# Kernel optimization log

Measured on AMD Instinct MI355X. Metric: run time of the kernel, lower is better.

## Reference

```python
import jax, jax.numpy as jnp
import numpy as np

N_EMBD = 1024
N_HEAD = 16

def setup_inputs() -> dict:
    key = jax.random.key(0)
    ks = jax.random.split(key, 6)
    C = N_EMBD
    s = 1.0 / np.sqrt(C)
    x = jax.random.normal(ks[0], (4, 2048, C), dtype=jnp.float32)
    Wk = jax.random.normal(ks[1], (C, C), dtype=jnp.float32) * s
    Wq = jax.random.normal(ks[2], (C, C), dtype=jnp.float32) * s
    Wv = jax.random.normal(ks[3], (C, C), dtype=jnp.float32) * s
    Wp = jax.random.normal(ks[4], (C, C), dtype=jnp.float32) * s
    bp = jax.random.normal(ks[5], (C,), dtype=jnp.float32) * 0.01
    return {"x": x, "Wq": Wq, "Wk": Wk, "Wv": Wv, "Wp": Wp, "bp": bp}

def reference(x, Wq, Wk, Wv, Wp, bp):
    B, T, C = x.shape
    H = N_HEAD
    d = C // H
    # projections (bias=False)
    q = (x @ Wq).reshape(B, T, H, d).transpose(0, 2, 1, 3)  # [B,H,T,d]
    k = (x @ Wk).reshape(B, T, H, d).transpose(0, 2, 1, 3)
    v = (x @ Wv).reshape(B, T, H, d).transpose(0, 2, 1, 3)
    att = jnp.einsum('bhqd,bhkd->bhqk', q, k) * (1.0 / np.sqrt(d))
    causal = jnp.tril(jnp.ones((T, T), dtype=bool))
    att = jnp.where(causal[None, None], att, jnp.float32(-jnp.inf))
    att = jax.nn.softmax(att, axis=-1)
    y = jnp.einsum('bhqk,bhkd->bhqd', att, v)  # [B,H,T,d]
    y = y.transpose(0, 2, 1, 3).reshape(B, T, C)
    return y @ Wp + bp
```

## Files before the change

### kernel.cpp

```cpp
#include <hip/hip_runtime.h>
#include <hip/hip_bf16.h>

#define N_EMBD 1024
#define N_HEADS 16
#define HD 64
#define TSEQ 2048
#define BATCH 4
#define M_TOT (BATCH*TSEQ)

typedef short s16x8 __attribute__((ext_vector_type(8)));
typedef float f32x4 __attribute__((ext_vector_type(4)));

__device__ __forceinline__ void glds16(const void* g, void* l) {
  __builtin_amdgcn_global_load_lds((const __attribute__((address_space(1))) void*)g,
                                   (__attribute__((address_space(3))) void*)l, 16, 0, 0);
}

__device__ __forceinline__ float exp_scaled(float s) {
  float r;
  asm("v_exp_f32 %0, %1\n\ts_nop 0" : "=v"(r) : "v"(s * 0.18033688011112042f));
  return r;
}

__device__ __forceinline__ unsigned cvtpk(float lo, float hi) {
  unsigned r;
  asm("v_cvt_pk_bf16_f32 %0, %1, %2" : "=v"(r) : "v"(lo), "v"(hi));
  return r;
}

__global__ __launch_bounds__(256) void xcast_kernel(const float* __restrict__ x,
                                                    __hip_bfloat16* __restrict__ xb) {
  int i = blockIdx.x * 256 + threadIdx.x;
  float4 f = ((const float4*)x)[i];
  __hip_bfloat162 p0, p1;
  p0.x = __float2bfloat16(f.x); p0.y = __float2bfloat16(f.y);
  p1.x = __float2bfloat16(f.z); p1.y = __float2bfloat16(f.w);
  ((__hip_bfloat162*)xb)[2*i]   = p0;
  ((__hip_bfloat162*)xb)[2*i+1] = p1;
}

__global__ void wcast_kernel(const float* __restrict__ Wq, const float* __restrict__ Wk,
                             const float* __restrict__ Wv, const float* __restrict__ Wp,
                             __hip_bfloat16* __restrict__ wqkvt, __hip_bfloat16* __restrict__ wpt) {
  __shared__ float tile[32][33];
  int z = blockIdx.z;
  const float* in = (z==0)?Wq:(z==1)?Wk:(z==2)?Wv:Wp;
  __hip_bfloat16* out = (z<3) ? (wqkvt + (size_t)z*N_EMBD*N_EMBD) : wpt;
  int tx = threadIdx.x, ty = threadIdx.y;
  int x  = blockIdx.x*32 + tx;
  int y0 = blockIdx.y*32;
  #pragma unroll
  for (int j=0;j<4;++j) tile[ty + j*8][tx] = in[(size_t)(y0+ty+j*8)*N_EMBD + x];
  __syncthreads();
  int xo  = y0 + tx;
  int yo0 = blockIdx.x*32;
  #pragma unroll
  for (int j=0;j<4;++j)
    out[(size_t)(yo0+ty+j*8)*N_EMBD + xo] = __float2bfloat16(tile[tx][ty+j*8]);
}

__global__ __launch_bounds__(256) void gemm_kernel(
    const __hip_bfloat16* __restrict__ A,
    const __hip_bfloat16* __restrict__ Bt,
    __hip_bfloat16* __restrict__ Qb, __hip_bfloat16* __restrict__ Kb,
    __hip_bfloat16* __restrict__ Vt,
    float* __restrict__ out, const float* __restrict__ bias, int mode) {
  __shared__ __align__(16) char smem[32768];
  __hip_bfloat16* Alin = (__hip_bfloat16*)smem;
  __hip_bfloat16* Blin = (__hip_bfloat16*)(smem + 16384);
  int tid = threadIdx.x;
  int m0 = blockIdx.y*128, n0 = blockIdx.x*128;
  int w = tid>>6, lane = tid&63, l16 = lane&15, quad = lane>>4;
  int wr = w>>1, wc = w&1;
  int xg = l16 & 7;
  int off0 = ((quad    ) ^ xg)*8;
  int off1 = ((quad + 4) ^ xg)*8;
  f32x4 acc[4][4];
  #pragma unroll
  for (int mi=0;mi<4;++mi)
    #pragma unroll
    for (int ni=0;ni<4;++ni) acc[mi][ni] = (f32x4){0.f,0.f,0.f,0.f};

  for (int k0=0; k0<N_EMBD; k0+=64) {
    __syncthreads();
    #pragma unroll
    for (int rd=0; rd<4; ++rd) {
      int slot = rd*256 + tid;
      int row  = slot>>3;
      int gc8  = ((tid&7) ^ (row&7))*8;
      glds16(A  + (size_t)(m0+row)*N_EMBD + k0 + gc8, Alin + slot*8);
      glds16(Bt + (size_t)(n0+row)*N_EMBD + k0 + gc8, Blin + slot*8);
    }
    __syncthreads();
    #pragma unroll
    for (int c=0;c<2;++c) {
      int off = c ? off1 : off0;
      s16x8 af[4], bfr[4];
      #pragma unroll
      for (int mi=0;mi<4;++mi)
        af[mi] = *(const s16x8*)(Alin + (wr*64+mi*16+l16)*64 + off);
      #pragma unroll
      for (int ni=0;ni<4;++ni)
        bfr[ni] = *(const s16x8*)(Blin + (wc*64+ni*16+l16)*64 + off);
      #pragma unroll
      for (int mi=0;mi<4;++mi)
        #pragma unroll
        for (int ni=0;ni<4;++ni)
          acc[mi][ni] = __builtin_amdgcn_mfma_f32_16x16x32_bf16(af[mi], bfr[ni], acc[mi][ni],0,0,0);
    }
  }

  if (mode == 0) {
    int which = n0 >> 10;
    int bb = m0 >> 11, t0 = m0 & 2047;
    if (which < 2) {
      __hip_bfloat16* outp = (which==0)?Qb:Kb;
      #pragma unroll
      for (int mi=0;mi<4;++mi) {
        #pragma unroll
        for (int ni=0;ni<4;++ni) {
          int ncol = (n0 & 1023) + wc*64 + ni*16 + l16;
          int hh = ncol>>6, dd = ncol&63;
          #pragma unroll
          for (int r=0;r<4;++r) {
            int t = t0 + wr*64 + mi*16 + quad*4 + r;
            outp[((size_t)(bb*N_HEADS + hh)*TSEQ + t)*HD + dd] = __float2bfloat16(acc[mi][ni][r]);
          }
        }
      }
    } else {
      int hh0 = (n0 & 1023) >> 6;
      __hip_bfloat16 (*Ts)[136] = (__hip_bfloat16(*)[136])smem;
      #pragma unroll
      for (int p=0;p<2;++p) {
        __syncthreads();
        if (wc == p) {
          #pragma unroll
          for (int mi=0;mi<4;++mi)
            #pragma unroll
            for (int ni=0;ni<4;++ni) {
              int dd = ni*16 + l16;
              #pragma unroll
              for (int r=0;r<4;++r)
                Ts[dd][wr*64 + mi*16 + quad*4 + r] = __float2bfloat16(acc[mi][ni][r]);
            }
        }
        __syncthreads();
        int dd = tid>>2, tc = (tid&3)*32;
        __hip_bfloat16* dst = Vt + ((size_t)(bb*N_HEADS + hh0 + p)*HD + dd)*TSEQ + t0;
        #pragma unroll
        for (int pb=0; pb<8; ++pb) {
          int q  = tc + pb*4;
          int pp = q & 63;
          int key = (q & 64) | (pp & 32) | ((pp & 4) << 2) | ((pp & 24) >> 1);
          *(uint2*)(dst + q) = *(const uint2*)&Ts[dd][key];
        }
      }
    }
  } else {
    #pragma unroll
    for (int mi=0;mi<4;++mi) {
      #pragma unroll
      for (int ni=0;ni<4;++ni) {
        int col = n0 + wc*64 + ni*16 + l16;
        float bs = bias[col];
        #pragma unroll
        for (int r=0;r<4;++r) {
          int m = m0 + wr*64 + mi*16 + quad*4 + r;
          out[(size_t)m*N_EMBD + col] = acc[mi][ni][r] + bs;
        }
      }
    }
  }
}

__global__ __launch_bounds__(256) void attn_kernel(
    const __hip_bfloat16* __restrict__ Qb, const __hip_bfloat16* __restrict__ Kb,
    const __hip_bfloat16* __restrict__ Vt, __hip_bfloat16* __restrict__ Yb) {
  __shared__ __align__(16) __hip_bfloat16 Ks[2][64][64];
  __shared__ __align__(16) __hip_bfloat16 Vs[2][64][64];
  int tid = threadIdx.x;
  int wgid = blockIdx.x;
  int qb = (int)((0x01237564AB89CDEFull >> ((wgid>>6)*4)) & 15);
  int h  = (wgid>>2) & 15;
  int b  = wgid & 3;
  int q0 = qb*128;
  size_t bhT  = (size_t)(b*N_HEADS + h)*TSEQ;
  size_t bhHD = (size_t)(b*N_HEADS + h)*HD;
  int lane = tid&63, w = tid>>6, l16 = lane&15, quad = lane>>4;
  int wq = w*32;
  int xg = l16 & 7;
  int off0 = ((quad    ) ^ xg)*8;
  int off1 = ((quad + 4) ^ xg)*8;

  int slot0 = tid,        row0 = slot0>>3, gcA = ((tid&7) ^ (row0&7))*8;
  int slot1 = 256 + tid,  row1 = slot1>>3, gcB = ((tid&7) ^ (row1&7))*8;

  s16x8 qf[2][2];
  #pragma unroll
  for (int mi=0;mi<2;++mi) {
    const __hip_bfloat16* qrow = Qb + (bhT + q0 + wq + mi*16 + l16)*HD;
    qf[mi][0] = *(const s16x8*)(qrow + quad*8);
    qf[mi][1] = *(const s16x8*)(qrow + 32 + quad*8);
  }

  f32x4 z4 = {0.f,0.f,0.f,0.f};
  f32x4 oacc[4][2];
  #pragma unroll
  for (int nd=0;nd<4;++nd) { oacc[nd][0]=z4; oacc[nd][1]=z4; }
  float lsum[2] = {0.f, 0.f};

  int ntiles = 2*qb + 2;

  {
    glds16(Kb + (bhT + 0 + row0)*HD + gcA,    &Ks[0][0][0] + slot0*8);
    glds16(Vt + (bhHD + row0)*TSEQ + 0 + gcA, &Vs[0][0][0] + slot0*8);
    glds16(Kb + (bhT + 0 + row1)*HD + gcB,    &Ks[0][0][0] + slot1*8);
    glds16(Vt + (bhHD + row1)*TSEQ + 0 + gcB, &Vs[0][0][0] + slot1*8);
  }

  for (int t=0; t<ntiles; ++t) {
    int cur = t&1;
    int k0 = t*64;
    if (t+1 < ntiles) {
      int kn = k0 + 64;
      glds16(Kb + (bhT + kn + row0)*HD + gcA,     &Ks[cur^1][0][0] + slot0*8);
      glds16(Vt + (bhHD + row0)*TSEQ + kn + gcA,  &Vs[cur^1][0][0] + slot0*8);
      glds16(Kb + (bhT + kn + row1)*HD + gcB,     &Ks[cur^1][0][0] + slot1*8);
      glds16(Vt + (bhHD + row1)*TSEQ + kn + gcB,  &Vs[cur^1][0][0] + slot1*8);
      asm volatile("s_waitcnt vmcnt(4)" ::: "memory");
    } else {
      asm volatile("s_waitcnt vmcnt(0)" ::: "memory");
    }
    __builtin_amdgcn_s_barrier();
    __builtin_amdgcn_sched_barrier(0);

    const __hip_bfloat16* Kc = &Ks[cur][0][0];
    const __hip_bfloat16* Vc = &Vs[cur][0][0];

    f32x4 sacc[4][2];
    #pragma unroll
    for (int ni=0; ni<4; ++ni) {
      s16x8 kb0 = *(const s16x8*)(Kc + (ni*16+l16)*64 + off0);
      s16x8 kb1 = *(const s16x8*)(Kc + (ni*16+l16)*64 + off1);
      #pragma unroll
      for (int mi=0; mi<2; ++mi) {
        f32x4 s = z4;
        s = __builtin_amdgcn_mfma_f32_16x16x32_bf16(kb0, qf[mi][0], s,0,0,0);
        s = __builtin_amdgcn_mfma_f32_16x16x32_bf16(kb1, qf[mi][1], s,0,0,0);
        sacc[ni][mi] = s;
      }
    }

    unsigned pkw[2][4][2];
    if (q0 + wq >= k0 + 63) {
      #pragma unroll
      for (int ni=0; ni<4; ++ni) {
        #pragma unroll
        for (int mi=0; mi<2; ++mi) {
          float e0 = exp_scaled(sacc[ni][mi][0]);
          float e1 = exp_scaled(sacc[ni][mi][1]);
          float e2 = exp_scaled(sacc[ni][mi][2]);
          float e3 = exp_scaled(sacc[ni][mi][3]);
          lsum[mi] += (e0+e1)+(e2+e3);
          pkw[mi][ni][0] = cvtpk(e0, e1);
          pkw[mi][ni][1] = cvtpk(e2, e3);
        }
      }
    } else {
      #pragma unroll
      for (int ni=0; ni<4; ++ni) {
        int kbase = k0 + ni*16 + quad*4;
        #pragma unroll
        for (int mi=0; mi<2; ++mi) {
          int qrow = q0 + wq + mi*16 + l16;
          float e0 = (qrow >= kbase    ) ? exp_scaled(sacc[ni][mi][0]) : 0.f;
          float e1 = (qrow >= kbase + 1) ? exp_scaled(sacc[ni][mi][1]) : 0.f;
          float e2 = (qrow >= kbase + 2) ? exp_scaled(sacc[ni][mi][2]) : 0.f;
          float e3 = (qrow >= kbase + 3) ? exp_scaled(sacc[ni][mi][3]) : 0.f;
          lsum[mi] += (e0+e1)+(e2+e3);
          pkw[mi][ni][0] = cvtpk(e0, e1);
          pkw[mi][ni][1] = cvtpk(e2, e3);
        }
      }
    }

    union U8 { s16x8 v; unsigned u[4]; };
    U8 pf[2][2];
    #pragma unroll
    for (int c=0; c<2; ++c)
      #pragma unroll
      for (int mi=0; mi<2; ++mi) {
        pf[c][mi].u[0] = pkw[mi][2*c  ][0];
        pf[c][mi].u[1] = pkw[mi][2*c  ][1];
        pf[c][mi].u[2] = pkw[mi][2*c+1][0];
        pf[c][mi].u[3] = pkw[mi][2*c+1][1];
      }
    #pragma unroll
    for (int nd=0; nd<4; ++nd) {
      const __hip_bfloat16* vrow = Vc + (nd*16 + l16)*64;
      s16x8 vb0 = *(const s16x8*)(vrow + off0);
      s16x8 vb1 = *(const s16x8*)(vrow + off1);
      oacc[nd][0] = __builtin_amdgcn_mfma_f32_16x16x32_bf16(vb0, pf[0][0].v, oacc[nd][0],0,0,0);
      oacc[nd][1] = __builtin_amdgcn_mfma_f32_16x16x32_bf16(vb0, pf[0][1].v, oacc[nd][1],0,0,0);
      oacc[nd][0] = __builtin_amdgcn_mfma_f32_16x16x32_bf16(vb1, pf[1][0].v, oacc[nd][0],0,0,0);
      oacc[nd][1] = __builtin_amdgcn_mfma_f32_16x16x32_bf16(vb1, pf[1][1].v, oacc[nd][1],0,0,0);
    }

    asm volatile("s_waitcnt lgkmcnt(0)" ::: "memory");
    __builtin_amdgcn_s_barrier();
    __builtin_amdgcn_sched_barrier(0);
  }

  #pragma unroll
  for (int mi=0; mi<2; ++mi) {
    lsum[mi] += __shfl_xor(lsum[mi], 16);
    lsum[mi] += __shfl_xor(lsum[mi], 32);
  }

  #pragma unroll
  for (int mi=0; mi<2; ++mi) {
    float inv = 1.f / lsum[mi];
    int tq = q0 + wq + mi*16 + l16;
    __hip_bfloat16* yr = Yb + ((size_t)(b*TSEQ + tq))*N_EMBD + h*HD + quad*4;
    #pragma unroll
    for (int nd=0; nd<4; ++nd) {
      uint2 o;
      o.x = cvtpk(oacc[nd][mi][0]*inv, oacc[nd][mi][1]*inv);
      o.y = cvtpk(oacc[nd][mi][2]*inv, oacc[nd][mi][3]*inv);
      *(uint2*)(yr + nd*16) = o;
    }
  }
}

extern "C" void kernel_launch(void* const* d_in, const int* in_sizes, int n_in,
                              void* d_out, int out_size, void* d_ws, size_t ws_size,
                              hipStream_t stream) {
  const float* x  = (const float*)d_in[0];
  const float* Wq = (const float*)d_in[1];
  const float* Wk = (const float*)d_in[2];
  const float* Wv = (const float*)d_in[3];
  const float* Wp = (const float*)d_in[4];
  const float* bp = (const float*)d_in[5];

  char* w = (char*)d_ws;
  __hip_bfloat16* xb    = (__hip_bfloat16*)w;  w += (size_t)M_TOT*N_EMBD*2;
  __hip_bfloat16* wqkvt = (__hip_bfloat16*)w;  w += (size_t)3*N_EMBD*N_EMBD*2;
  __hip_bfloat16* wpt   = (__hip_bfloat16*)w;  w += (size_t)N_EMBD*N_EMBD*2;
  __hip_bfloat16* Qb    = (__hip_bfloat16*)w;  w += (size_t)M_TOT*N_EMBD*2;
  __hip_bfloat16* Kb    = (__hip_bfloat16*)w;  w += (size_t)M_TOT*N_EMBD*2;
  __hip_bfloat16* Vt    = (__hip_bfloat16*)w;  w += (size_t)M_TOT*N_EMBD*2;
  __hip_bfloat16* Yb    = (__hip_bfloat16*)w;

  xcast_kernel<<<dim3(M_TOT*N_EMBD/1024), dim3(256), 0, stream>>>(x, xb);
  wcast_kernel<<<dim3(32,32,4), dim3(32,8), 0, stream>>>(Wq,Wk,Wv,Wp,wqkvt,wpt);
  gemm_kernel<<<dim3(24,64), dim3(256), 0, stream>>>(xb, wqkvt, Qb,Kb,Vt, nullptr, nullptr, 0);
  attn_kernel<<<dim3(1024), dim3(256), 0, stream>>>(Qb,Kb,Vt,Yb);
  gemm_kernel<<<dim3(8,64), dim3(256), 0, stream>>>(Yb, wpt, nullptr,nullptr,nullptr,
                                                    (float*)d_out, bp, 1);
}
```

Before: 239.2 us.

## Remap GEMM blocks per XCD and stage Q/K epilogue through LDS

Blocks are renumbered so that consecutive workgroups, which the hardware spreads round-robin over the eight XCDs, map to contiguous N-column ranges on each XCD. The aim is better L2 reuse of the B operand. The Q/K epilogue now transposes the accumulator tile through shared memory and writes 16-byte vectorized rows, replacing scattered 2-byte stores. This adds two barriers per head half, and the remap assumes gridDim.x is divisible by 8.

```diff
diff --git a/kernel.cpp b/kernel.cpp
--- a/kernel.cpp
+++ b/kernel.cpp
@@ -69,7 +69,12 @@
   __hip_bfloat16* Alin = (__hip_bfloat16*)smem;
   __hip_bfloat16* Blin = (__hip_bfloat16*)(smem + 16384);
   int tid = threadIdx.x;
-  int m0 = blockIdx.y*128, n0 = blockIdx.x*128;
+  int wg  = blockIdx.x + gridDim.x*blockIdx.y;
+  int per = gridDim.x >> 3;
+  int xcd = wg & 7, idx = wg >> 3;
+  int bxn = xcd*per + (idx % per);
+  int byn = idx / per;
+  int m0 = byn*128, n0 = bxn*128;
   int w = tid>>6, lane = tid&63, l16 = lane&15, quad = lane>>4;
   int wr = w>>1, wc = w&1;
   int xg = l16 & 7;
@@ -115,18 +120,29 @@
     int bb = m0 >> 11, t0 = m0 & 2047;
     if (which < 2) {
       __hip_bfloat16* outp = (which==0)?Qb:Kb;
-      #pragma unroll
-      for (int mi=0;mi<4;++mi) {
-        #pragma unroll
-        for (int ni=0;ni<4;++ni) {
-          int ncol = (n0 & 1023) + wc*64 + ni*16 + l16;
-          int hh = ncol>>6, dd = ncol&63;
+      int hh0 = (n0 & 1023) >> 6;
+      __hip_bfloat16 (*Tq)[68] = (__hip_bfloat16(*)[68])smem;
+      #pragma unroll
+      for (int p=0;p<2;++p) {
+        __syncthreads();
+        if (wc == p) {
           #pragma unroll
-          for (int r=0;r<4;++r) {
-            int t = t0 + wr*64 + mi*16 + quad*4 + r;
-            outp[((size_t)(bb*N_HEADS + hh)*TSEQ + t)*HD + dd] = __float2bfloat16(acc[mi][ni][r]);
-          }
-        }
+          for (int mi=0;mi<4;++mi)
+            #pragma unroll
+            for (int ni=0;ni<4;++ni) {
+              int col = ni*16 + l16;
+              int rbase = wr*64 + mi*16 + quad*4;
+              #pragma unroll
+              for (int r=0;r<4;++r)
+                Tq[rbase + r][col] = __float2bfloat16(acc[mi][ni][r]);
+            }
+        }
+        __syncthreads();
+        int row = tid>>1, half = (tid&1)*32;
+        __hip_bfloat16* dst = outp + ((size_t)(bb*N_HEADS + hh0 + p)*TSEQ + t0 + row)*HD + half;
+        #pragma unroll
+        for (int c4=0;c4<4;++c4)
+          *(uint4*)(dst + c4*8) = *(const uint4*)&Tq[row][half + c4*8];
       }
     } else {
       int hh0 = (n0 & 1023) >> 6;
```

Result: slower. 246.1 us (+2.9%).

## Add 256x256-tile double-buffered QKV GEMM kernel with 8 waves

Applied to the files above, without the earlier changes.

Replaces the 128x128-tile QKV projection GEMM with a new kernel that computes 256x256 output tiles using 512 threads. It double-buffers 128 KB of LDS, prefetches with global_load_lds interleaved across four quadrant MFMA phases, and uses explicit waitcnt, barriers and setprio. The larger tile raises arithmetic intensity and overlaps loads with compute. In exchange, LDS use caps occupancy at one block per CU and the grid shrinks to 384 blocks. The Q/K/V scatter epilogues are ported to the new tile shape and removed from the old kernel.

```diff
diff --git a/kernel.cpp b/kernel.cpp
--- a/kernel.cpp
+++ b/kernel.cpp
@@ -57,6 +57,172 @@
   #pragma unroll
   for (int j=0;j<4;++j)
     out[(size_t)(yo0+ty+j*8)*N_EMBD + xo] = __float2bfloat16(tile[tx][ty+j*8]);
+}
+
+__global__ __launch_bounds__(512, 2) void gemm256_kernel(
+    const __hip_bfloat16* __restrict__ A,
+    const __hip_bfloat16* __restrict__ Bt,
+    __hip_bfloat16* __restrict__ Qb, __hip_bfloat16* __restrict__ Kb,
+    __hip_bfloat16* __restrict__ Vt) {
+  __shared__ __align__(16) char smem[131072];
+  int tid = threadIdx.x;
+  int nb = blockIdx.x;
+  int m0 = blockIdx.y * 256;
+  const __hip_bfloat16* Asrc = A  + (size_t)m0 * N_EMBD;
+  const __hip_bfloat16* Bsrc = Bt + (size_t)nb * 256 * N_EMBD;
+
+  int lane = tid & 63, wv = tid >> 6, l16 = lane & 15, quad = lane >> 4;
+  int swr = wv >> 2, swc = wv & 3;
+  int xg = l16 & 7;
+  int offc0 = ((quad    ) ^ xg) * 8;
+  int offc1 = ((quad + 4) ^ xg) * 8;
+  int r0  = tid >> 3;
+  int gsw = ((tid & 7) ^ (r0 & 7)) * 8;
+  int gln = (tid & 7) * 8;
+
+  f32x4 acc[2][2][4][2];
+  #pragma unroll
+  for (int a=0;a<2;++a)
+    #pragma unroll
+    for (int b=0;b<2;++b)
+      #pragma unroll
+      for (int c=0;c<4;++c)
+        #pragma unroll
+        for (int d=0;d<2;++d) acc[a][b][c][d] = (f32x4){0.f,0.f,0.f,0.f};
+
+#define STG(srcbase, kk, hh_, dst_) do {                                      \
+    const __hip_bfloat16* s_ = (srcbase) + (size_t)((hh_)*128 + r0)*N_EMBD + (kk) + gsw; \
+    __hip_bfloat16* d_ = (dst_) + (hh_)*8192 + r0*64 + gln;                   \
+    glds16(s_, d_);                                                           \
+    glds16(s_ + (size_t)64*N_EMBD, d_ + 64*64);                               \
+  } while (0)
+#define RDA(qm_) do { _Pragma("unroll") for (int mi=0;mi<4;++mi) {            \
+    const __hip_bfloat16* p_ = Acur + ((qm_)*128 + swr*64 + mi*16 + l16)*64;  \
+    af[mi][0] = *(const s16x8*)(p_ + offc0);                                  \
+    af[mi][1] = *(const s16x8*)(p_ + offc1); } } while (0)
+#define RDB(qn_) do { _Pragma("unroll") for (int ni=0;ni<2;++ni) {            \
+    const __hip_bfloat16* p_ = Bcur + ((qn_)*128 + swc*32 + ni*16 + l16)*64;  \
+    bq[ni][0] = *(const s16x8*)(p_ + offc0);                                  \
+    bq[ni][1] = *(const s16x8*)(p_ + offc1); } } while (0)
+#define MM(qm_,qn_) do { _Pragma("unroll") for (int mi=0;mi<4;++mi)           \
+    _Pragma("unroll") for (int ni=0;ni<2;++ni) {                              \
+      acc[qm_][qn_][mi][ni] = __builtin_amdgcn_mfma_f32_16x16x32_bf16(af[mi][0], bq[ni][0], acc[qm_][qn_][mi][ni],0,0,0); \
+      acc[qm_][qn_][mi][ni] = __builtin_amdgcn_mfma_f32_16x16x32_bf16(af[mi][1], bq[ni][1], acc[qm_][qn_][mi][ni],0,0,0); } } while (0)
+
+  {
+    __hip_bfloat16* A0b = (__hip_bfloat16*)smem;
+    __hip_bfloat16* B0b = (__hip_bfloat16*)(smem + 32768);
+    STG(Asrc, 0, 0, A0b);
+    STG(Bsrc, 0, 0, B0b);
+    STG(Asrc, 0, 1, A0b);
+    STG(Bsrc, 0, 1, B0b);
+  }
+
+  for (int t = 0; t < 16; ++t) {
+    int kn = t*64 + 64;
+    char* cb   = smem + (size_t)(t & 1) * 65536;
+    char* nbuf = smem + (size_t)((t + 1) & 1) * 65536;
+    const __hip_bfloat16* Acur = (const __hip_bfloat16*)cb;
+    const __hip_bfloat16* Bcur = (const __hip_bfloat16*)(cb + 32768);
+    __hip_bfloat16* An = (__hip_bfloat16*)nbuf;
+    __hip_bfloat16* Bn = (__hip_bfloat16*)(nbuf + 32768);
+    bool pf = (t < 15);
+    s16x8 af[4][2], bq[2][2];
+
+    if (pf) { STG(Asrc, kn, 0, An); asm volatile("s_waitcnt vmcnt(6)" ::: "memory"); }
+    else    {                       asm volatile("s_waitcnt vmcnt(4)" ::: "memory"); }
+    __builtin_amdgcn_s_barrier();
+    __builtin_amdgcn_sched_barrier(0);
+    RDA(0); RDB(0);
+    asm volatile("s_waitcnt lgkmcnt(0)" ::: "memory");
+    __builtin_amdgcn_sched_barrier(0);
+    __builtin_amdgcn_s_setprio(1); MM(0,0); __builtin_amdgcn_s_setprio(0);
+
+    if (pf) { STG(Bsrc, kn, 0, Bn); asm volatile("s_waitcnt vmcnt(6)" ::: "memory"); }
+    else    {                       asm volatile("s_waitcnt vmcnt(2)" ::: "memory"); }
+    __builtin_amdgcn_s_barrier();
+    __builtin_amdgcn_sched_barrier(0);
+    RDA(1);
+    asm volatile("s_waitcnt lgkmcnt(0)" ::: "memory");
+    __builtin_amdgcn_sched_barrier(0);
+    __builtin_amdgcn_s_setprio(1); MM(1,0); __builtin_amdgcn_s_setprio(0);
+
+    if (pf) { STG(Asrc, kn, 1, An); asm volatile("s_waitcnt vmcnt(6)" ::: "memory"); }
+    else    {                       asm volatile("s_waitcnt vmcnt(0)" ::: "memory"); }
+    __builtin_amdgcn_s_barrier();
+    __builtin_amdgcn_sched_barrier(0);
+    RDB(1);
+    asm volatile("s_waitcnt lgkmcnt(0)" ::: "memory");
+    __builtin_amdgcn_sched_barrier(0);
+    __builtin_amdgcn_s_setprio(1); MM(1,1); __builtin_amdgcn_s_setprio(0);
+
+    if (pf) STG(Bsrc, kn, 1, Bn);
+    RDA(0);
+    asm volatile("s_waitcnt lgkmcnt(0)" ::: "memory");
+    __builtin_amdgcn_s_barrier();
+    __builtin_amdgcn_sched_barrier(0);
+    __builtin_amdgcn_s_setprio(1); MM(0,1); __builtin_amdgcn_s_setprio(0);
+  }
+#undef STG
+#undef RDA
+#undef RDB
+#undef MM
+
+  int which = nb >> 2;
+  int bb = m0 >> 11, t0 = m0 & 2047;
+  if (which < 2) {
+    __hip_bfloat16* outp = (which==0)?Qb:Kb;
+    int nloc = (nb & 3) * 256;
+    #pragma unroll
+    for (int qm=0;qm<2;++qm)
+      #pragma unroll
+      for (int qn=0;qn<2;++qn)
+        #pragma unroll
+        for (int mi=0;mi<4;++mi)
+          #pragma unroll
+          for (int ni=0;ni<2;++ni) {
+            int col = nloc + qn*128 + swc*32 + ni*16 + l16;
+            int hh = col >> 6, dd = col & 63;
+            int trow = t0 + qm*128 + swr*64 + mi*16 + quad*4;
+            __hip_bfloat16* dst = outp + ((size_t)(bb*N_HEADS + hh)*TSEQ + trow)*HD + dd;
+            #pragma unroll
+            for (int r=0;r<4;++r)
+              dst[(size_t)r*HD] = __float2bfloat16(acc[qm][qn][mi][ni][r]);
+          }
+  } else {
+    int hh0 = (nb & 3) * 4;
+    __hip_bfloat16 (*Ts)[264] = (__hip_bfloat16(*)[264])smem;
+    #pragma unroll
+    for (int hd=0; hd<4; ++hd) {
+      if (hd) __builtin_amdgcn_s_barrier();
+      if ((swc >> 1) == (hd & 1)) {
+        int qn = hd >> 1;
+        int ddb = (swc & 1) * 32;
+        #pragma unroll
+        for (int qm=0;qm<2;++qm)
+          #pragma unroll
+          for (int mi=0;mi<4;++mi)
+            #pragma unroll
+            for (int ni=0;ni<2;++ni) {
+              int dd = ddb + ni*16 + l16;
+              int trow = qm*128 + swr*64 + mi*16 + quad*4;
+              #pragma unroll
+              for (int r=0;r<4;++r)
+                Ts[dd][trow + r] = __float2bfloat16(acc[qm][qn][mi][ni][r]);
+            }
+      }
+      __syncthreads();
+      int dd = tid >> 3, tcb = (tid & 7) * 32;
+      __hip_bfloat16* dst = Vt + ((size_t)(bb*N_HEADS + hh0 + hd)*HD + dd)*TSEQ + t0;
+      #pragma unroll
+      for (int pb=0; pb<8; ++pb) {
+        int q  = tcb + pb*4;
+        int pp = q & 63;
+        int key = (q & 192) | (pp & 32) | ((pp & 4) << 2) | ((pp & 24) >> 1);
+        *(uint2*)(dst + q) = *(const uint2*)&Ts[dd][key];
+      }
+    }
+  }
 }
 
 __global__ __launch_bounds__(256) void gemm_kernel(
@@ -111,52 +277,6 @@
   }
 
   if (mode == 0) {
-    int which = n0 >> 10;
-    int bb = m0 >> 11, t0 = m0 & 2047;
-    if (which < 2) {
-      __hip_bfloat16* outp = (which==0)?Qb:Kb;
-      #pragma unroll
-      for (int mi=0;mi<4;++mi) {
-        #pragma unroll
-        for (int ni=0;ni<4;++ni) {
-          int ncol = (n0 & 1023) + wc*64 + ni*16 + l16;
-          int hh = ncol>>6, dd = ncol&63;
-          #pragma unroll
-          for (int r=0;r<4;++r) {
-            int t = t0 + wr*64 + mi*16 + quad*4 + r;
-            outp[((size_t)(bb*N_HEADS + hh)*TSEQ + t)*HD + dd] = __float2bfloat16(acc[mi][ni][r]);
-          }
-        }
-      }
-    } else {
-      int hh0 = (n0 & 1023) >> 6;
-      __hip_bfloat16 (*Ts)[136] = (__hip_bfloat16(*)[136])smem;
-      #pragma unroll
-      for (int p=0;p<2;++p) {
-        __syncthreads();
-        if (wc == p) {
-          #pragma unroll
-          for (int mi=0;mi<4;++mi)
-            #pragma unroll
-            for (int ni=0;ni<4;++ni) {
-              int dd = ni*16 + l16;
-              #pragma unroll
-              for (int r=0;r<4;++r)
-                Ts[dd][wr*64 + mi*16 + quad*4 + r] = __float2bfloat16(acc[mi][ni][r]);
-            }
-        }
-        __syncthreads();
-        int dd = tid>>2, tc = (tid&3)*32;
-        __hip_bfloat16* dst = Vt + ((size_t)(bb*N_HEADS + hh0 + p)*HD + dd)*TSEQ + t0;
-        #pragma unroll
-        for (int pb=0; pb<8; ++pb) {
-          int q  = tc + pb*4;
-          int pp = q & 63;
-          int key = (q & 64) | (pp & 32) | ((pp & 4) << 2) | ((pp & 24) >> 1);
-          *(uint2*)(dst + q) = *(const uint2*)&Ts[dd][key];
-        }
-      }
-    }
   } else {
     #pragma unroll
     for (int mi=0;mi<4;++mi) {
@@ -354,7 +474,7 @@
 
   xcast_kernel<<<dim3(M_TOT*N_EMBD/1024), dim3(256), 0, stream>>>(x, xb);
   wcast_kernel<<<dim3(32,32,4), dim3(32,8), 0, stream>>>(Wq,Wk,Wv,Wp,wqkvt,wpt);
-  gemm_kernel<<<dim3(24,64), dim3(256), 0, stream>>>(xb, wqkvt, Qb,Kb,Vt, nullptr, nullptr, 0);
+  gemm256_kernel<<<dim3(12,32), dim3(512), 0, stream>>>(xb, wqkvt, Qb,Kb,Vt);
   attn_kernel<<<dim3(1024), dim3(256), 0, stream>>>(Qb,Kb,Vt,Yb);
   gemm_kernel<<<dim3(8,64), dim3(256), 0, stream>>>(Yb, wpt, nullptr,nullptr,nullptr,
                                                     (float*)d_out, bp, 1);
```

After: 238.5 us. No clear change (-0.3%).
